# Optimization experiments

Hardware: AMD Instinct MI355X
Metric: run time of the kernel (lower is better)

## Reference

```python
import jax, jax.numpy as jnp
import numpy as np

VOCAB = 50000; T = 4096; EMBED = 500; H = 500  # hidden per direction (HIDDEN_SIZE=1000, bidirectional)
NUM_TAGS = 16; START = 14; STOP = 15
NEG = -10000.0


def setup_inputs() -> dict:
    key = jax.random.key(0)
    ks = jax.random.split(key, 16)
    n = lambda k, s, sc=0.1: (jax.random.normal(k, s) * sc).astype(jnp.float32)
    trans = n(ks[12], (NUM_TAGS, NUM_TAGS), 1.0)
    trans = trans.at[START, :].set(NEG).at[:, STOP].set(NEG)  # as in __init__
    return {
        "sent": jax.random.randint(ks[0], (T,), 0, VOCAB),
        "embed_w": n(ks[1], (VOCAB, EMBED), 1.0),
        "wih0": n(ks[2], (2, 4 * H, EMBED)),
        "whh0": n(ks[3], (2, 4 * H, H)),
        "bih0": n(ks[4], (2, 4 * H)),
        "bhh0": n(ks[5], (2, 4 * H)),
        "wih1": n(ks[6], (2, 4 * H, 2 * H)),
        "whh1": n(ks[7], (2, 4 * H, H)),
        "bih1": n(ks[8], (2, 4 * H)),
        "bhh1": n(ks[9], (2, 4 * H)),
        "w_out": n(ks[10], (NUM_TAGS, 2 * H)),
        "b_out": n(ks[11], (NUM_TAGS,)),
        "trans": trans,
        "h0": n(ks[13], (4, H), 1.0),  # init_hidden() uses randn; layout [layer*2+dir, H]
        "c0": n(ks[14], (4, H), 1.0),
    }


def _lstm_dir(x, wih, whh, bih, bhh, h0, c0):
    b = bih + bhh
    def cell(carry, xt):
        h, c = carry
        g = xt @ wih.T + h @ whh.T + b          # [4H], torch gate order i,f,g,o
        i, f, gg, o = jnp.split(g, 4)
        c = jax.nn.sigmoid(f) * c + jax.nn.sigmoid(i) * jnp.tanh(gg)
        h = jax.nn.sigmoid(o) * jnp.tanh(c)
        return (h, c), h
    _, hs = jax.lax.scan(cell, (h0, c0), x)
    return hs  # [T, H]


def _bilstm_layer(x, wih, whh, bih, bhh, h0, c0):
    fwd = _lstm_dir(x, wih[0], whh[0], bih[0], bhh[0], h0[0], c0[0])
    bwd = _lstm_dir(x[::-1], wih[1], whh[1], bih[1], bhh[1], h0[1], c0[1])[::-1]
    return jnp.concatenate([fwd, bwd], axis=-1)  # [T, 2H]


def _features(sent, embed_w, wih0, whh0, bih0, bhh0, wih1, whh1, bih1, bhh1, w_out, b_out, h0, c0):
    x = embed_w[sent]                                            # [T, EMBED]
    x = _bilstm_layer(x, wih0, whh0, bih0, bhh0, h0[0:2], c0[0:2])
    x = _bilstm_layer(x, wih1, whh1, bih1, bhh1, h0[2:4], c0[2:4])
    return x @ w_out.T + b_out                                   # [T, NUM_TAGS]


def _viterbi(feats, trans):
    score0 = jnp.full((NUM_TAGS,), NEG, dtype=feats.dtype).at[START].set(0.0)
    def step(score, feat):
        m = score[None, :] + trans               # m[tag, prev] = score[prev] + trans[tag, prev]
        return jnp.max(m, axis=1) + feat, jnp.argmax(m, axis=1)
    score, bptr = jax.lax.scan(step, score0, feats)              # bptr: [T, NUM_TAGS]
    score = score + trans[STOP]
    best_tag = jnp.argmax(score)
    best_score = score[best_tag]
    # faithful to the source backtrace: best_tag is NOT updated inside its loop,
    # so path = [bptr[1][bt], ..., bptr[T-1][bt], bt]
    path = jnp.concatenate([bptr[1:, best_tag], best_tag[None]])
    return best_score, path


def reference(sent, embed_w, wih0, whh0, bih0, bhh0, wih1, whh1, bih1, bhh1, w_out, b_out, trans, h0, c0):
    feats = _features(sent, embed_w, wih0, whh0, bih0, bhh0,
                      wih1, whh1, bih1, bhh1, w_out, b_out, h0, c0)
    return _viterbi(feats, trans)
```

## Files before the change

### kernel.cpp

```cpp
#include <hip/hip_runtime.h>


#define T_SEQ 4096
#define HPAD  512
#define NTAG  16


__global__ void zero_k(float* __restrict__ p, int n) {
  int i = blockIdx.x * blockDim.x + threadIdx.x;
  int stride = gridDim.x * blockDim.x;
  for (; i < n; i += stride) p[i] = 0.0f;
}

__global__ void embed_k(const int* __restrict__ sent, const float* __restrict__ ew,
                        float* __restrict__ x0) {
  int t = blockIdx.x;
  int row = sent[t];
  for (int k = threadIdx.x; k < HPAD; k += blockDim.x)
    x0[(size_t)t * HPAD + k] = (k < 500) ? ew[(size_t)row * 500 + k] : 0.0f;
}

__global__ __launch_bounds__(256) void gin_gemm_k(
    const float* __restrict__ A, int KA,
    const float* __restrict__ wih, const float* __restrict__ bih,
    const float* __restrict__ bhh, int Kreal, float* __restrict__ G) {
  const int dir = blockIdx.z;
  const int bm = blockIdx.y, bn = blockIdx.x;
  const float* W = wih + (size_t)dir * 2000 * Kreal;

  __shared__ float As[16][128];
  __shared__ float Bs[16][128];

  const int tid = threadIdx.x;
  const int tx = tid & 15, ty = tid >> 4;
  float acc[8][8] = {};

  for (int k0 = 0; k0 < KA; k0 += 16) {
#pragma unroll
    for (int q = 0; q < 2; q++) {
      int f4 = tid + q * 256;
      int m = f4 >> 2, kc = (f4 & 3) * 4;
      float4 av = *reinterpret_cast<const float4*>(A + (size_t)(bm * 128 + m) * KA + k0 + kc);
      As[kc + 0][m] = av.x; As[kc + 1][m] = av.y;
      As[kc + 2][m] = av.z; As[kc + 3][m] = av.w;
    }
#pragma unroll
    for (int q = 0; q < 2; q++) {
      int f4 = tid + q * 256;
      int n = f4 >> 2, kc = (f4 & 3) * 4;
      int nn = bn * 128 + n;
      int gate = nn >> 9, j = nn & 511;
#pragma unroll
      for (int e = 0; e < 4; e++) {
        int k = k0 + kc + e;
        int jk = k & 511, half = k >> 9;
        float v = 0.0f;
        if (j < 500 && jk < 500)
          v = W[(size_t)(gate * 500 + j) * Kreal + half * 500 + jk];
        Bs[kc + e][n] = v;
      }
    }
    __syncthreads();
#pragma unroll
    for (int kk = 0; kk < 16; kk++) {
      float a[8], b[8];
      *reinterpret_cast<float4*>(&a[0]) = *reinterpret_cast<const float4*>(&As[kk][ty * 8]);
      *reinterpret_cast<float4*>(&a[4]) = *reinterpret_cast<const float4*>(&As[kk][ty * 8 + 4]);
      *reinterpret_cast<float4*>(&b[0]) = *reinterpret_cast<const float4*>(&Bs[kk][tx * 8]);
      *reinterpret_cast<float4*>(&b[4]) = *reinterpret_cast<const float4*>(&Bs[kk][tx * 8 + 4]);
#pragma unroll
      for (int i = 0; i < 8; i++)
#pragma unroll
        for (int j = 0; j < 8; j++) acc[i][j] = fmaf(a[i], b[j], acc[i][j]);
    }
    __syncthreads();
  }
#pragma unroll
  for (int i = 0; i < 8; i++) {
#pragma unroll
    for (int j = 0; j < 8; j++) {
      int m = bm * 128 + ty * 8 + i;
      int nn = bn * 128 + tx * 8 + j;
      int gate = nn >> 9, ju = nn & 511;
      float o = 0.0f;
      if (ju < 500) {
        int r = gate * 500 + ju;
        o = acc[i][j] + bih[dir * 2000 + r] + bhh[dir * 2000 + r];
      }
      G[((size_t)dir * T_SEQ + m) * 2048 + nn] = o;
    }
  }
}

__device__ __forceinline__ unsigned long long pack_hv(unsigned tag, float h) {
  return (unsigned long long)tag | ((unsigned long long)__float_as_uint(h) << 32);
}

__global__ void hinit_k(const float* __restrict__ h0, int layer,
                        unsigned long long* __restrict__ hcomm) {
  int i = blockIdx.x * blockDim.x + threadIdx.x;
  int dir = i >> 10, par = (i >> 9) & 1, j = i & 511;
  unsigned long long v;
  if (par == 0) {
    float h = (j < 500) ? h0[(layer * 2 + dir) * 500 + j] : 0.0f;
    v = pack_hv(0u, h);
  } else {
    v = 0xFFFFFFFFull;
  }
  hcomm[(size_t)(dir * 2 + par) * HPAD + j] = v;
}

__global__ __launch_bounds__(1024)
__attribute__((amdgpu_waves_per_eu(4, 4)))
void lstm_k(
    const float* __restrict__ whh_base,
    const float* __restrict__ gin,
    const float* __restrict__ c0,
    float* __restrict__ xout,
    unsigned long long* __restrict__ hcomm,
    int layer) {
  __shared__ float part[16][68];
  __shared__ float hbuf[16][32];

  const int tid = threadIdx.x;
  const int dir = blockIdx.x >> 5;
  const int wgd = blockIdx.x & 31;
  const int w = tid >> 6;
  const int lane = tid & 63;

  const int gate = lane >> 4;
  const int ul   = lane & 15;
  const int j    = wgd * 16 + ul;
  const int row  = gate * 500 + j;

  float wreg[32];
  const float* Wd = whh_base + (size_t)dir * 2000 * 500;
#pragma unroll
  for (int i = 0; i < 32; i++) {
    int k = w * 32 + i;
    wreg[i] = (j < 500 && k < 500) ? Wd[(size_t)row * 500 + k] : 0.0f;
  }
#pragma unroll
  for (int i = 0; i < 32; i++) asm volatile("" : "+v"(wreg[i]));

  float c = 0.0f;
  if (w == 0 && lane < 16 && j < 500) c = c0[(layer * 2 + dir) * 500 + j];

  unsigned long long* hcd = hcomm + (size_t)dir * 2 * HPAD;
  bool dead = false;

  for (int t = 0; t < T_SEQ; t++) {
    const int t_in = (dir == 0) ? t : (T_SEQ - 1 - t);

    float gi = 0.0f;
    if (w == 0) {
      const float* gb = gin + ((size_t)dir * T_SEQ + t_in) * 2048;
      gi = gb[gate * 512 + j];
    }

    unsigned long long v = 0;
    if (!dead) {
      const unsigned long long* hp =
          hcd + (size_t)(t & 1) * HPAD + w * 32 + (lane & 31);
      int guard = 0;
      for (;;) {
        v = __hip_atomic_load(hp, __ATOMIC_RELAXED, __HIP_MEMORY_SCOPE_AGENT);
        if (__all((int)((unsigned)v == (unsigned)t))) break;
        if (++guard > (1 << 22)) { dead = true; break; }
      }
    }
    float hval = __uint_as_float((unsigned)(v >> 32));

    if (lane < 32) hbuf[w][lane] = hval;
    float a = 0.0f;
#pragma unroll
    for (int b = 0; b < 8; b++) {
      float4 hv = *reinterpret_cast<const float4*>(&hbuf[w][b * 4]);
      a = fmaf(wreg[b * 4 + 0], hv.x, a);
      a = fmaf(wreg[b * 4 + 1], hv.y, a);
      a = fmaf(wreg[b * 4 + 2], hv.z, a);
      a = fmaf(wreg[b * 4 + 3], hv.w, a);
    }
    part[w][lane] = a;
    __syncthreads();

    if (w == 0) {
      float s = gi;
#pragma unroll
      for (int q = 0; q < 16; q++) s += part[q][lane];
      float nl = (gate == 2) ? tanhf(s) : (1.0f / (1.0f + expf(-s)));
      float xf = __shfl(nl, lane + 16, 64);
      float xg = __shfl(nl, lane + 32, 64);
      float xo = __shfl(nl, lane + 48, 64);
      if (lane < 16) {
        c = xf * c + nl * xg;
        float h = xo * tanhf(c);
        unsigned long long sv = pack_hv((unsigned)(t + 1), h);
        __hip_atomic_store(hcd + (size_t)((t + 1) & 1) * HPAD + j, sv,
                           __ATOMIC_RELAXED, __HIP_MEMORY_SCOPE_AGENT);
        if (j < 500)
          xout[(size_t)t_in * 1024 + (size_t)dir * HPAD + j] = h;
      }
    }
  }
}

__global__ __launch_bounds__(256) void feats_k(
    const float* __restrict__ x2, const float* __restrict__ w_out,
    const float* __restrict__ b_out, float* __restrict__ feats) {
  int tid = threadIdx.x;
  int tag = tid & 15, tl = tid >> 4;
  int t = blockIdx.x * 16 + tl;
  float acc = 0.0f;
  for (int k = 0; k < 1024; k++) {
    int jk = k & 511;
    if (jk < 500)
      acc = fmaf(x2[(size_t)t * 1024 + k], w_out[tag * 1000 + (k >> 9) * 500 + jk], acc);
  }
  feats[t * 16 + tag] = acc + b_out[tag];
}

__global__ __launch_bounds__(256) void viterbi_k(
    const float* __restrict__ feats, const float* __restrict__ trans,
    int* __restrict__ bptr, float* __restrict__ out) {
  __shared__ float sfin[NTAG];
  __shared__ int sbest;
  int tid = threadIdx.x;
  if (tid < 64) {
    int tag = tid & 15;
    float treg[16];
#pragma unroll
    for (int p = 0; p < 16; p++) treg[p] = trans[tag * 16 + p];
    float s = (tag == 14) ? 0.0f : -10000.0f;
    for (int t = 0; t < T_SEQ; t++) {
      float best = -3.4e38f;
      int barg = 0;
#pragma unroll
      for (int p = 0; p < 16; p++) {
        float cand = __shfl(s, p, 16) + treg[p];
        if (cand > best) { best = cand; barg = p; }
      }
      s = best + feats[t * 16 + tag];
      if (tid < 16) bptr[t * 16 + tag] = barg;
    }
    s += trans[15 * 16 + tag];
    if (tid < 16) sfin[tag] = s;
  }
  __syncthreads();
  if (tid == 0) {
    float best = -3.4e38f;
    int bt = 0;
    for (int p = 0; p < 16; p++) {
      float vv = sfin[p];
      if (vv > best) { best = vv; bt = p; }
    }
    out[0] = best;
    sbest = bt;
  }
  __syncthreads();
  int bt = sbest;
  for (int i = tid; i < T_SEQ - 1; i += blockDim.x)
    out[1 + i] = (float)bptr[(i + 1) * 16 + bt];
  if (tid == 0) out[T_SEQ] = (float)bt;
}

extern "C" void kernel_launch(void* const* d_in, const int* in_sizes, int n_in,
                              void* d_out, int out_size, void* d_ws, size_t ws_size,
                              hipStream_t stream) {
  const int*   sent  = (const int*)d_in[0];
  const float* embed = (const float*)d_in[1];
  const float* wih0  = (const float*)d_in[2];
  const float* whh0  = (const float*)d_in[3];
  const float* bih0  = (const float*)d_in[4];
  const float* bhh0  = (const float*)d_in[5];
  const float* wih1  = (const float*)d_in[6];
  const float* whh1  = (const float*)d_in[7];
  const float* bih1  = (const float*)d_in[8];
  const float* bhh1  = (const float*)d_in[9];
  const float* w_out = (const float*)d_in[10];
  const float* b_out = (const float*)d_in[11];
  const float* trans = (const float*)d_in[12];
  const float* h0    = (const float*)d_in[13];
  const float* c0    = (const float*)d_in[14];
  float* out = (float*)d_out;

  char* ws = (char*)d_ws;
  float* x0    = (float*)(ws + 0);
  float* x1    = (float*)(ws + 8388608);
  float* x2    = (float*)(ws + 25165824);
  float* gin   = (float*)(ws + 41943040);
  float* feats = (float*)(ws + 109051904);
  int*   bptr  = (int*)(ws + 109314048);
  unsigned long long* hcomm = (unsigned long long*)(ws + 109576192);

  zero_k<<<2048, 256, 0, stream>>>(x1, 2 * T_SEQ * 1024);
  embed_k<<<T_SEQ, 256, 0, stream>>>(sent, embed, x0);

  gin_gemm_k<<<dim3(16, 32, 2), 256, 0, stream>>>(x0, 512, wih0, bih0, bhh0, 500, gin);
  hinit_k<<<2, 1024, 0, stream>>>(h0, 0, hcomm);
  lstm_k<<<64, 1024, 0, stream>>>(whh0, gin, c0, x1, hcomm, 0);

  gin_gemm_k<<<dim3(16, 32, 2), 256, 0, stream>>>(x1, 1024, wih1, bih1, bhh1, 1000, gin);
  hinit_k<<<2, 1024, 0, stream>>>(h0, 1, hcomm);
  lstm_k<<<64, 1024, 0, stream>>>(whh1, gin, c0, x2, hcomm, 1);

  feats_k<<<T_SEQ / 16, 256, 0, stream>>>(x2, w_out, b_out, feats);
  viterbi_k<<<1, 256, 0, stream>>>(feats, trans, bptr, out);
}
```

Measured before the change: 15.24 ms.

## Halve LSTM workgroup waves and replace barrier with LDS flag handoff

The recurrent LSTM kernel now runs with 8 waves per workgroup instead of 16, each wave holding 64 weight registers covering 64 hidden inputs. The per-step __syncthreads is replaced by double-buffered partial sums in LDS plus per-wave flags that only wave 0 spins on, so the producer waves can move on to polling the next step's hidden state without waiting at a full barrier. This aims to cut barrier latency on the serial time-step critical path. In exchange each wave does twice the FMAs per step, register pressure rises, and correctness now depends on the hand-written waitcnt and flag ordering in LDS.

Result: slower. 16.51 ms (+8.3%).

```diff
diff --git a/kernel.cpp b/kernel.cpp
--- a/kernel.cpp
+++ b/kernel.cpp
@@ -110,8 +110,8 @@
   hcomm[(size_t)(dir * 2 + par) * HPAD + j] = v;
 }
 
-__global__ __launch_bounds__(1024)
-__attribute__((amdgpu_waves_per_eu(4, 4)))
+__global__ __launch_bounds__(512)
+__attribute__((amdgpu_waves_per_eu(2, 4)))
 void lstm_k(
     const float* __restrict__ whh_base,
     const float* __restrict__ gin,
@@ -119,8 +119,9 @@
     float* __restrict__ xout,
     unsigned long long* __restrict__ hcomm,
     int layer) {
-  __shared__ float part[16][68];
-  __shared__ float hbuf[16][32];
+  __shared__ float part[2][8][68];
+  __shared__ int   flags[2][8];
+  __shared__ float hbuf[8][64];
 
   const int tid = threadIdx.x;
   const int dir = blockIdx.x >> 5;
@@ -133,15 +134,18 @@
   const int j    = wgd * 16 + ul;
   const int row  = gate * 500 + j;
 
-  float wreg[32];
+  if (tid < 16) ((int*)flags)[tid] = -1;
+  __syncthreads();
+
+  float wreg[64];
   const float* Wd = whh_base + (size_t)dir * 2000 * 500;
 #pragma unroll
-  for (int i = 0; i < 32; i++) {
-    int k = w * 32 + i;
+  for (int i = 0; i < 64; i++) {
+    int k = w * 64 + i;
     wreg[i] = (j < 500 && k < 500) ? Wd[(size_t)row * 500 + k] : 0.0f;
   }
 #pragma unroll
-  for (int i = 0; i < 32; i++) asm volatile("" : "+v"(wreg[i]));
+  for (int i = 0; i < 64; i++) asm volatile("" : "+v"(wreg[i]));
 
   float c = 0.0f;
   if (w == 0 && lane < 16 && j < 500) c = c0[(layer * 2 + dir) * 500 + j];
@@ -151,6 +155,7 @@
 
   for (int t = 0; t < T_SEQ; t++) {
     const int t_in = (dir == 0) ? t : (T_SEQ - 1 - t);
+    const int p = t & 1;
 
     float gi = 0.0f;
     if (w == 0) {
@@ -160,8 +165,7 @@
 
     unsigned long long v = 0;
     if (!dead) {
-      const unsigned long long* hp =
-          hcd + (size_t)(t & 1) * HPAD + w * 32 + (lane & 31);
+      const unsigned long long* hp = hcd + (size_t)p * HPAD + w * 64 + lane;
       int guard = 0;
       for (;;) {
         v = __hip_atomic_load(hp, __ATOMIC_RELAXED, __HIP_MEMORY_SCOPE_AGENT);
@@ -171,23 +175,38 @@
     }
     float hval = __uint_as_float((unsigned)(v >> 32));
 
-    if (lane < 32) hbuf[w][lane] = hval;
+    hbuf[w][lane] = hval;
     float a = 0.0f;
 #pragma unroll
-    for (int b = 0; b < 8; b++) {
+    for (int b = 0; b < 16; b++) {
       float4 hv = *reinterpret_cast<const float4*>(&hbuf[w][b * 4]);
       a = fmaf(wreg[b * 4 + 0], hv.x, a);
       a = fmaf(wreg[b * 4 + 1], hv.y, a);
       a = fmaf(wreg[b * 4 + 2], hv.z, a);
       a = fmaf(wreg[b * 4 + 3], hv.w, a);
     }
-    part[w][lane] = a;
-    __syncthreads();
-
-    if (w == 0) {
-      float s = gi;
-#pragma unroll
-      for (int q = 0; q < 16; q++) s += part[q][lane];
+
+    if (w > 0) {
+      part[p][w][lane] = a;
+      asm volatile("s_waitcnt lgkmcnt(0)" ::: "memory");
+      if (lane == 0)
+        __hip_atomic_store(&flags[p][w], t, __ATOMIC_RELAXED,
+                           __HIP_MEMORY_SCOPE_WORKGROUP);
+    } else {
+      if (!dead) {
+        const bool need = (lane >= 1 && lane < 8);
+        const int fq = need ? lane : 0;
+        int guard = 0;
+        for (;;) {
+          int fv = __hip_atomic_load(&flags[p][fq], __ATOMIC_RELAXED,
+                                     __HIP_MEMORY_SCOPE_WORKGROUP);
+          if (__all(!need || (fv == t))) break;
+          if (++guard > (1 << 22)) { dead = true; break; }
+        }
+      }
+      float s = gi + a;
+#pragma unroll
+      for (int q = 1; q < 8; q++) s += part[p][q][lane];
       float nl = (gate == 2) ? tanhf(s) : (1.0f / (1.0f + expf(-s)));
       float xf = __shfl(nl, lane + 16, 64);
       float xg = __shfl(nl, lane + 32, 64);
@@ -298,11 +317,11 @@
 
   gin_gemm_k<<<dim3(16, 32, 2), 256, 0, stream>>>(x0, 512, wih0, bih0, bhh0, 500, gin);
   hinit_k<<<2, 1024, 0, stream>>>(h0, 0, hcomm);
-  lstm_k<<<64, 1024, 0, stream>>>(whh0, gin, c0, x1, hcomm, 0);
+  lstm_k<<<64, 512, 0, stream>>>(whh0, gin, c0, x1, hcomm, 0);
 
   gin_gemm_k<<<dim3(16, 32, 2), 256, 0, stream>>>(x1, 1024, wih1, bih1, bhh1, 1000, gin);
   hinit_k<<<2, 1024, 0, stream>>>(h0, 1, hcomm);
-  lstm_k<<<64, 1024, 0, stream>>>(whh1, gin, c0, x2, hcomm, 1);
+  lstm_k<<<64, 512, 0, stream>>>(whh1, gin, c0, x2, hcomm, 1);
 
   feats_k<<<T_SEQ / 16, 256, 0, stream>>>(x2, w_out, b_out, feats);
   viterbi_k<<<1, 256, 0, stream>>>(feats, trans, bptr, out);
```

## Interleave both LSTM directions per workgroup, prepack input weights, use fast activations

Applied to the files above, without the earlier changes.

The recurrent kernel now runs both directions in each workgroup on 32 blocks instead of 64. It alternates forward and backward steps so that one direction's cross-block spin wait overlaps with the other's compute. The input-projection GEMM now reads a pre-packed, padded weight matrix and bias through float4 loads instead of doing gathered, bounds-checked loads. Sigmoid and tanh use __expf with a hardware reciprocal. This doubles register pressure for the recurrent weights, adds packing kernels that reuse the x2 and bptr scratch buffers, and slightly reduces activation accuracy.

Measured after the change: 18.99 ms. +24.6%, slower.

```diff
diff --git a/kernel.cpp b/kernel.cpp
--- a/kernel.cpp
+++ b/kernel.cpp
@@ -20,13 +20,34 @@
     x0[(size_t)t * HPAD + k] = (k < 500) ? ew[(size_t)row * 500 + k] : 0.0f;
 }
 
+__global__ __launch_bounds__(256) void wpack_k(
+    const float* __restrict__ wih, const float* __restrict__ bih,
+    const float* __restrict__ bhh, int Kreal, int KAp,
+    float* __restrict__ Wp, float* __restrict__ bp) {
+  const int n = blockIdx.x;
+  const int dir = blockIdx.y;
+  const int gate = n >> 9, j = n & 511;
+  const int row = gate * 500 + j;
+  const float* W = wih + (size_t)dir * 2000 * Kreal;
+  float* dst = Wp + ((size_t)dir * 2048 + n) * KAp;
+  for (int k = threadIdx.x; k < KAp; k += 256) {
+    int half = k >> 9, jk = k & 511;
+    float v = 0.0f;
+    if (j < 500 && jk < 500)
+      v = W[(size_t)row * Kreal + half * 500 + jk];
+    dst[k] = v;
+  }
+  if (threadIdx.x == 0)
+    bp[dir * 2048 + n] = (j < 500) ? bih[dir * 2000 + row] + bhh[dir * 2000 + row] : 0.0f;
+}
+
 __global__ __launch_bounds__(256) void gin_gemm_k(
     const float* __restrict__ A, int KA,
-    const float* __restrict__ wih, const float* __restrict__ bih,
-    const float* __restrict__ bhh, int Kreal, float* __restrict__ G) {
+    const float* __restrict__ Wp, const float* __restrict__ bp,
+    float* __restrict__ G) {
   const int dir = blockIdx.z;
   const int bm = blockIdx.y, bn = blockIdx.x;
-  const float* W = wih + (size_t)dir * 2000 * Kreal;
+  const float* W = Wp + (size_t)dir * 2048 * KA;
 
   __shared__ float As[16][128];
   __shared__ float Bs[16][128];
@@ -48,17 +69,9 @@
     for (int q = 0; q < 2; q++) {
       int f4 = tid + q * 256;
       int n = f4 >> 2, kc = (f4 & 3) * 4;
-      int nn = bn * 128 + n;
-      int gate = nn >> 9, j = nn & 511;
-#pragma unroll
-      for (int e = 0; e < 4; e++) {
-        int k = k0 + kc + e;
-        int jk = k & 511, half = k >> 9;
-        float v = 0.0f;
-        if (j < 500 && jk < 500)
-          v = W[(size_t)(gate * 500 + j) * Kreal + half * 500 + jk];
-        Bs[kc + e][n] = v;
-      }
+      float4 bv = *reinterpret_cast<const float4*>(W + (size_t)(bn * 128 + n) * KA + k0 + kc);
+      Bs[kc + 0][n] = bv.x; Bs[kc + 1][n] = bv.y;
+      Bs[kc + 2][n] = bv.z; Bs[kc + 3][n] = bv.w;
     }
     __syncthreads();
 #pragma unroll
@@ -81,19 +94,21 @@
     for (int j = 0; j < 8; j++) {
       int m = bm * 128 + ty * 8 + i;
       int nn = bn * 128 + tx * 8 + j;
-      int gate = nn >> 9, ju = nn & 511;
-      float o = 0.0f;
-      if (ju < 500) {
-        int r = gate * 500 + ju;
-        o = acc[i][j] + bih[dir * 2000 + r] + bhh[dir * 2000 + r];
-      }
-      G[((size_t)dir * T_SEQ + m) * 2048 + nn] = o;
+      G[((size_t)dir * T_SEQ + m) * 2048 + nn] = acc[i][j] + bp[dir * 2048 + nn];
     }
   }
 }
 
 __device__ __forceinline__ unsigned long long pack_hv(unsigned tag, float h) {
   return (unsigned long long)tag | ((unsigned long long)__float_as_uint(h) << 32);
+}
+
+__device__ __forceinline__ float fsig(float x) {
+  float e = __expf(-x);
+  return __builtin_amdgcn_rcpf(1.0f + e);
+}
+__device__ __forceinline__ float ftanhf(float x) {
+  return fmaf(2.0f, fsig(x + x), -1.0f);
 }
 
 __global__ void hinit_k(const float* __restrict__ h0, int layer,
@@ -119,12 +134,11 @@
     float* __restrict__ xout,
     unsigned long long* __restrict__ hcomm,
     int layer) {
-  __shared__ float part[16][68];
+  __shared__ float part[2][16][68];
   __shared__ float hbuf[16][32];
 
   const int tid = threadIdx.x;
-  const int dir = blockIdx.x >> 5;
-  const int wgd = blockIdx.x & 31;
+  const int wgd = blockIdx.x;
   const int w = tid >> 6;
   const int lane = tid & 63;
 
@@ -133,73 +147,127 @@
   const int j    = wgd * 16 + ul;
   const int row  = gate * 500 + j;
 
-  float wreg[32];
-  const float* Wd = whh_base + (size_t)dir * 2000 * 500;
+  float wreg0[32], wreg1[32];
 #pragma unroll
   for (int i = 0; i < 32; i++) {
     int k = w * 32 + i;
-    wreg[i] = (j < 500 && k < 500) ? Wd[(size_t)row * 500 + k] : 0.0f;
-  }
-#pragma unroll
-  for (int i = 0; i < 32; i++) asm volatile("" : "+v"(wreg[i]));
-
-  float c = 0.0f;
-  if (w == 0 && lane < 16 && j < 500) c = c0[(layer * 2 + dir) * 500 + j];
-
-  unsigned long long* hcd = hcomm + (size_t)dir * 2 * HPAD;
-  bool dead = false;
+    bool ok = (j < 500 && k < 500);
+    wreg0[i] = ok ? whh_base[(size_t)row * 500 + k] : 0.0f;
+    wreg1[i] = ok ? whh_base[(size_t)(2000 + row) * 500 + k] : 0.0f;
+  }
+#pragma unroll
+  for (int i = 0; i < 32; i++) {
+    asm volatile("" : "+v"(wreg0[i]));
+    asm volatile("" : "+v"(wreg1[i]));
+  }
+
+  float cA = 0.0f, cB = 0.0f;
+  if (w == 0 && lane < 16 && j < 500) {
+    cA = c0[(layer * 2 + 0) * 500 + j];
+    cB = c0[(layer * 2 + 1) * 500 + j];
+  }
+
+  unsigned long long* hc0 = hcomm;
+  unsigned long long* hc1 = hcomm + 2 * HPAD;
+  bool dead0 = false, dead1 = false;
 
   for (int t = 0; t < T_SEQ; t++) {
-    const int t_in = (dir == 0) ? t : (T_SEQ - 1 - t);
-
-    float gi = 0.0f;
+    const int p = t & 1;
+    const int t0_in = t;
+    const int t1_in = T_SEQ - 1 - t;
+
+    const unsigned long long* hp0 = hc0 + (size_t)p * HPAD + w * 32 + (lane & 31);
+    const unsigned long long* hp1 = hc1 + (size_t)p * HPAD + w * 32 + (lane & 31);
+
+    unsigned long long v1 = 0;
+    if (!dead1) v1 = __hip_atomic_load(hp1, __ATOMIC_RELAXED, __HIP_MEMORY_SCOPE_AGENT);
+
+    float gi0 = 0.0f, gi1 = 0.0f;
     if (w == 0) {
-      const float* gb = gin + ((size_t)dir * T_SEQ + t_in) * 2048;
-      gi = gb[gate * 512 + j];
-    }
-
-    unsigned long long v = 0;
-    if (!dead) {
-      const unsigned long long* hp =
-          hcd + (size_t)(t & 1) * HPAD + w * 32 + (lane & 31);
+      gi0 = gin[((size_t)0 * T_SEQ + t0_in) * 2048 + gate * 512 + j];
+      gi1 = gin[((size_t)1 * T_SEQ + t1_in) * 2048 + gate * 512 + j];
+    }
+
+    unsigned long long v0 = 0;
+    if (!dead0) {
       int guard = 0;
       for (;;) {
-        v = __hip_atomic_load(hp, __ATOMIC_RELAXED, __HIP_MEMORY_SCOPE_AGENT);
-        if (__all((int)((unsigned)v == (unsigned)t))) break;
-        if (++guard > (1 << 22)) { dead = true; break; }
-      }
-    }
-    float hval = __uint_as_float((unsigned)(v >> 32));
-
-    if (lane < 32) hbuf[w][lane] = hval;
-    float a = 0.0f;
-#pragma unroll
-    for (int b = 0; b < 8; b++) {
-      float4 hv = *reinterpret_cast<const float4*>(&hbuf[w][b * 4]);
-      a = fmaf(wreg[b * 4 + 0], hv.x, a);
-      a = fmaf(wreg[b * 4 + 1], hv.y, a);
-      a = fmaf(wreg[b * 4 + 2], hv.z, a);
-      a = fmaf(wreg[b * 4 + 3], hv.w, a);
-    }
-    part[w][lane] = a;
+        v0 = __hip_atomic_load(hp0, __ATOMIC_RELAXED, __HIP_MEMORY_SCOPE_AGENT);
+        if (__all((int)((unsigned)v0 == (unsigned)t))) break;
+        if (++guard > (1 << 22)) { dead0 = true; break; }
+      }
+    }
+    {
+      float hval = __uint_as_float((unsigned)(v0 >> 32));
+      if (lane < 32) hbuf[w][lane] = hval;
+      float a = 0.0f;
+#pragma unroll
+      for (int b = 0; b < 8; b++) {
+        float4 hv = *reinterpret_cast<const float4*>(&hbuf[w][b * 4]);
+        a = fmaf(wreg0[b * 4 + 0], hv.x, a);
+        a = fmaf(wreg0[b * 4 + 1], hv.y, a);
+        a = fmaf(wreg0[b * 4 + 2], hv.z, a);
+        a = fmaf(wreg0[b * 4 + 3], hv.w, a);
+      }
+      part[0][w][lane] = a;
+    }
     __syncthreads();
-
     if (w == 0) {
-      float s = gi;
-#pragma unroll
-      for (int q = 0; q < 16; q++) s += part[q][lane];
-      float nl = (gate == 2) ? tanhf(s) : (1.0f / (1.0f + expf(-s)));
+      float s = gi0;
+#pragma unroll
+      for (int q = 0; q < 16; q++) s += part[0][q][lane];
+      float nl = (gate == 2) ? ftanhf(s) : fsig(s);
       float xf = __shfl(nl, lane + 16, 64);
       float xg = __shfl(nl, lane + 32, 64);
       float xo = __shfl(nl, lane + 48, 64);
       if (lane < 16) {
-        c = xf * c + nl * xg;
-        float h = xo * tanhf(c);
-        unsigned long long sv = pack_hv((unsigned)(t + 1), h);
-        __hip_atomic_store(hcd + (size_t)((t + 1) & 1) * HPAD + j, sv,
+        cA = xf * cA + nl * xg;
+        float h = xo * ftanhf(cA);
+        __hip_atomic_store(hc0 + (size_t)((t + 1) & 1) * HPAD + j,
+                           pack_hv((unsigned)(t + 1), h),
                            __ATOMIC_RELAXED, __HIP_MEMORY_SCOPE_AGENT);
-        if (j < 500)
-          xout[(size_t)t_in * 1024 + (size_t)dir * HPAD + j] = h;
+        if (j < 500) xout[(size_t)t0_in * 1024 + j] = h;
+      }
+    }
+
+    if (!dead1 && !__all((int)((unsigned)v1 == (unsigned)t))) {
+      int guard = 0;
+      for (;;) {
+        v1 = __hip_atomic_load(hp1, __ATOMIC_RELAXED, __HIP_MEMORY_SCOPE_AGENT);
+        if (__all((int)((unsigned)v1 == (unsigned)t))) break;
+        if (++guard > (1 << 22)) { dead1 = true; break; }
+      }
+    }
+    {
+      float hval = __uint_as_float((unsigned)(v1 >> 32));
+      if (lane < 32) hbuf[w][lane] = hval;
+      float a = 0.0f;
+#pragma unroll
+      for (int b = 0; b < 8; b++) {
+        float4 hv = *reinterpret_cast<const float4*>(&hbuf[w][b * 4]);
+        a = fmaf(wreg1[b * 4 + 0], hv.x, a);
+        a = fmaf(wreg1[b * 4 + 1], hv.y, a);
+        a = fmaf(wreg1[b * 4 + 2], hv.z, a);
+        a = fmaf(wreg1[b * 4 + 3], hv.w, a);
+      }
+      part[1][w][lane] = a;
+    }
+    __syncthreads();
+    if (w == 0) {
+      float s = gi1;
+#pragma unroll
+      for (int q = 0; q < 16; q++) s += part[1][q][lane];
+      float nl = (gate == 2) ? ftanhf(s) : fsig(s);
+      float xf = __shfl(nl, lane + 16, 64);
+      float xg = __shfl(nl, lane + 32, 64);
+      float xo = __shfl(nl, lane + 48, 64);
+      if (lane < 16) {
+        cB = xf * cB + nl * xg;
+        float h = xo * ftanhf(cB);
+        __hip_atomic_store(hc1 + (size_t)((t + 1) & 1) * HPAD + j,
+                           pack_hv((unsigned)(t + 1), h),
+                           __ATOMIC_RELAXED, __HIP_MEMORY_SCOPE_AGENT);
+        if (j < 500) xout[(size_t)t1_in * 1024 + HPAD + j] = h;
       }
     }
   }
@@ -292,17 +360,21 @@
   float* feats = (float*)(ws + 109051904);
   int*   bptr  = (int*)(ws + 109314048);
   unsigned long long* hcomm = (unsigned long long*)(ws + 109576192);
-
-  zero_k<<<2048, 256, 0, stream>>>(x1, 2 * T_SEQ * 1024);
+  float* Wp = x2;
+  float* bp = (float*)(ws + 109314048);
+
+  zero_k<<<1024, 256, 0, stream>>>(x1, T_SEQ * 1024);
   embed_k<<<T_SEQ, 256, 0, stream>>>(sent, embed, x0);
 
-  gin_gemm_k<<<dim3(16, 32, 2), 256, 0, stream>>>(x0, 512, wih0, bih0, bhh0, 500, gin);
+  wpack_k<<<dim3(2048, 2), 256, 0, stream>>>(wih0, bih0, bhh0, 500, 512, Wp, bp);
+  gin_gemm_k<<<dim3(16, 32, 2), 256, 0, stream>>>(x0, 512, Wp, bp, gin);
   hinit_k<<<2, 1024, 0, stream>>>(h0, 0, hcomm);
-  lstm_k<<<64, 1024, 0, stream>>>(whh0, gin, c0, x1, hcomm, 0);
-
-  gin_gemm_k<<<dim3(16, 32, 2), 256, 0, stream>>>(x1, 1024, wih1, bih1, bhh1, 1000, gin);
+  lstm_k<<<32, 1024, 0, stream>>>(whh0, gin, c0, x1, hcomm, 0);
+
+  wpack_k<<<dim3(2048, 2), 256, 0, stream>>>(wih1, bih1, bhh1, 1000, 1024, Wp, bp);
+  gin_gemm_k<<<dim3(16, 32, 2), 256, 0, stream>>>(x1, 1024, Wp, bp, gin);
   hinit_k<<<2, 1024, 0, stream>>>(h0, 1, hcomm);
-  lstm_k<<<64, 1024, 0, stream>>>(whh1, gin, c0, x2, hcomm, 1);
+  lstm_k<<<32, 1024, 0, stream>>>(whh1, gin, c0, x2, hcomm, 1);
 
   feats_k<<<T_SEQ / 16, 256, 0, stream>>>(x2, w_out, b_out, feats);
   viterbi_k<<<1, 256, 0, stream>>>(feats, trans, bptr, out);
```
